# Kernel optimization log

Measured on AMD Instinct MI355X. Metric: run time of the kernel, lower is better.

Reference implementation:

```python
import jax, jax.numpy as jnp
import numpy as np

D_MODEL = 768
N_HEADS = 24
D_HEAD = 64
D_STATE = 64
CHUNK = 64
D_INNER = N_HEADS * D_HEAD  # 1536
N_LAYER = 24
B_SZ = 2
SEQ = 8192
RMS_EPS = 1.1920929e-07  # torch.finfo(float32).eps (nn.RMSNorm default eps)


def setup_inputs() -> dict:
    key = jax.random.key(0)
    ks = jax.random.split(key, 8)
    proj = N_HEADS * (1 + 2 * D_STATE)
    return {
        "hidden_states": jax.random.normal(ks[0], (B_SZ, SEQ, D_MODEL), jnp.float32),
        "norm_w": jnp.ones((D_MODEL,), jnp.float32),
        "in_proj_w": jax.random.normal(ks[1], (2 * D_INNER, D_MODEL), jnp.float32) * 0.02,
        "in_proj_b": jnp.zeros((2 * D_INNER,), jnp.float32),
        "conv_w": jax.random.normal(ks[2], (D_INNER, 1, 4), jnp.float32) * 0.25,
        "conv_b": jnp.zeros((D_INNER,), jnp.float32),
        "x_proj_w": jax.random.normal(ks[3], (proj, D_INNER), jnp.float32) * 0.02,
        "x_proj_b": jnp.zeros((proj,), jnp.float32),
        "A_log": jnp.full((N_HEADS,), float(np.log(0.5)), jnp.float32),
        "log2_alpha_base": jnp.full((N_HEADS,), -0.15, jnp.float32),
        "log2_beta": jnp.zeros((N_HEADS,), jnp.float32),
        "surprise_ema": jnp.ones((N_HEADS,), jnp.float32),
        "out_proj_w": jax.random.normal(ks[4], (D_MODEL, D_INNER), jnp.float32) * 0.02,
        "out_proj_b": jnp.zeros((D_MODEL,), jnp.float32),
        "res_gate": jnp.full((1,), 1.0 / float(np.sqrt(2 * N_LAYER)), jnp.float32),
    }


def _block_forward(hidden_states, norm_w, in_proj_w, in_proj_b, conv_w, conv_b,
                   x_proj_w, x_proj_b, A_log, log2_alpha_base, log2_beta,
                   surprise_ema, out_proj_w, out_proj_b, res_gate):
    residual = hidden_states
    b, L, _ = hidden_states.shape

    # RMSNorm
    x = hidden_states * jax.lax.rsqrt(
        jnp.mean(hidden_states ** 2, axis=-1, keepdims=True) + RMS_EPS) * norm_w

    # in_proj, split x/z
    xz = hidden_states_proj = x @ in_proj_w.T + in_proj_b
    x, z = jnp.split(xz, 2, axis=-1)  # [b, L, d_inner] each

    # causal depthwise conv1d (kernel 4, padding 3, then truncate to L)
    xc = jnp.transpose(x, (0, 2, 1))  # [b, C, L]
    xc = jax.lax.conv_general_dilated(
        xc, conv_w, window_strides=(1,), padding=[(3, 3)],
        dimension_numbers=("NCH", "OIH", "NCH"), feature_group_count=D_INNER)
    xc = xc[:, :, :L] + conv_b[None, :, None]
    x = jax.nn.silu(jnp.transpose(xc, (0, 2, 1)))  # [b, L, d_inner]

    # x_proj -> dt, B, C
    xp = (x @ x_proj_w.T + x_proj_b).reshape(b, L, N_HEADS, 1 + 2 * D_STATE)
    dt = xp[..., 0]
    B_ssm = xp[..., 1:1 + D_STATE]
    C_ssm = xp[..., 1 + D_STATE:]
    B_ssm = B_ssm / jnp.maximum(jnp.linalg.norm(B_ssm, axis=-1, keepdims=True), 1e-12)
    C_ssm = C_ssm / jnp.maximum(jnp.linalg.norm(C_ssm, axis=-1, keepdims=True), 1e-12)

    A = jnp.clip(A_log, -2.3, -0.01)[None, None, :]  # [1,1,H]
    dt_scale = jnp.clip(jax.nn.softplus(jnp.clip(dt, -10.0, 10.0)), 0.01, 10.0)
    A = jnp.clip(A * dt_scale, -20.0, -0.001)  # [b, L, H]

    X = x.reshape(b, L, N_HEADS, D_HEAD)

    # ---- chunked surprise-gated SSD (L divisible by CHUNK) ----
    n = L // CHUNK
    X_t = X.reshape(b, n, CHUNK, N_HEADS, D_HEAD).transpose(0, 3, 1, 2, 4)      # b h n c d
    A_t = A.reshape(b, n, CHUNK, N_HEADS).transpose(0, 3, 1, 2)                 # b h n c
    B_t = B_ssm.reshape(b, n, CHUNK, N_HEADS, D_STATE).transpose(0, 3, 1, 2, 4) # b h n c s
    C_t = C_ssm.reshape(b, n, CHUNK, N_HEADS, D_STATE).transpose(0, 3, 1, 2, 4) # b h n c s

    BX = jnp.einsum("bhncs,bhncd->bhnsd", B_t, X_t)
    chunk_surprise = jnp.mean(BX ** 2, axis=(-1, -2))  # [b, h, n]

    # surprise gate (training=True: EMA updated first, no_grad)
    mean_s = jax.lax.stop_gradient(jnp.mean(chunk_surprise, axis=(0, 2)))
    ema = 0.99 * surprise_ema + 0.01 * mean_s
    normalized = chunk_surprise / (ema[None, :, None] + 1e-6)
    alpha_base = 1.0 - 2.0 ** jnp.clip(log2_alpha_base, -3.32, -0.015)  # [H]
    beta = 2.0 ** jnp.clip(log2_beta, -2.0, 2.0)                        # [H]
    boost_pos = jax.nn.relu(jnp.tanh(beta[None, :, None] * normalized))
    ab = alpha_base[None, :, None]
    alpha = jnp.clip(ab + (1.0 - ab) * boost_pos, 0.01, 0.999)          # [b, h, n]

    A_mod = A_t * (1.0 - alpha)[..., None]          # b h n c
    A_cs = jnp.cumsum(A_mod, axis=-1)               # b h n c

    # intra-chunk: L[i,j] = exp(cs_i - cs_j) for i >= j
    diff = A_cs[..., :, None] - A_cs[..., None, :]  # b h n c c
    mask = jnp.tril(jnp.ones((CHUNK, CHUNK), bool))
    Lmat = jnp.where(mask, jnp.exp(diff), 0.0)
    CB = jnp.einsum("bhnid,bhnjd->bhnij", C_t, B_t)
    Y_intra = jnp.einsum("bhnij,bhnjd->bhnid", Lmat * CB, X_t)

    # inter-chunk recurrence
    decay_chunk = jnp.exp(jnp.sum(A_mod, axis=-1))              # b h n
    decay_to_end = jnp.exp(A_cs[..., -1:] - A_cs)               # b h n c
    h_chunk_final = jnp.einsum("bhnc,bhncs,bhncd->bhnsd",
                               decay_to_end, B_t, X_t)           # b h n s d

    def step(carry, inp):
        d, hf = inp  # d: [b,h], hf: [b,h,s,d]
        new = d[..., None, None] * carry + hf
        return new, carry  # emit state BEFORE this chunk

    carry0 = jnp.zeros((b, N_HEADS, D_STATE, D_HEAD), X.dtype)
    _, h_inter = jax.lax.scan(
        step, carry0,
        (decay_chunk.transpose(2, 0, 1), h_chunk_final.transpose(2, 0, 1, 3, 4)))
    h_inter = h_inter.transpose(1, 2, 0, 3, 4)  # b h n s d

    decay_from_start = jnp.exp(A_cs)  # b h n c
    Y_inter = jnp.einsum("bhnis,bhnsp,bhni->bhnip", C_t, h_inter, decay_from_start)

    Y = (Y_intra + Y_inter).transpose(0, 2, 3, 1, 4).reshape(b, L, D_INNER)

    # gate + out proj + gated residual
    y = jnp.clip(Y, -100.0, 100.0) * jax.nn.sigmoid(z)
    out = jnp.clip(y @ out_proj_w.T + out_proj_b, -100.0, 100.0)
    return residual + out * res_gate


def reference(hidden_states, norm_w, in_proj_w, in_proj_b, conv_w, conv_b,
              x_proj_w, x_proj_b, A_log, log2_alpha_base, log2_beta,
              surprise_ema, out_proj_w, out_proj_b, res_gate):
    return _block_forward(hidden_states, norm_w, in_proj_w, in_proj_b, conv_w,
                          conv_b, x_proj_w, x_proj_b, A_log, log2_alpha_base,
                          log2_beta, surprise_ema, out_proj_w, out_proj_b, res_gate)
```

## Files before the change

### kernel.cpp

```cpp
#include <hip/hip_runtime.h>
#include <hip/hip_bf16.h>
#include <cstdint>
#include <cstddef>

#define L_SEQ   8192
#define DMODEL  768
#define NHEADS  24
#define DINNER  1536
#define NPROJ   3096
#define NPROJP  3200
#define NPROJ2  3264
#define HSTR    136
#define NTOK    16384
#define BT      8192
#define RMS_EPS 1.1920929e-07f

typedef __hip_bfloat16 bf16;
typedef __attribute__((ext_vector_type(8))) short bf8v;
typedef __attribute__((ext_vector_type(4))) float f4v;

__device__ __forceinline__ float clampf(float x, float lo, float hi) {
    return fminf(fmaxf(x, lo), hi);
}
__device__ __forceinline__ float bf2f(bf16 v) { return __bfloat162float(v); }
__device__ __forceinline__ bf16  f2bf(float v) { return __float2bfloat16(v); }
__device__ __forceinline__ short f2bs(float v) {
    bf16 b = __float2bfloat16(v);
    return *reinterpret_cast<short*>(&b);
}
__device__ __forceinline__ float bs2f(short v) {
    return __uint_as_float(((unsigned)(unsigned short)v) << 16);
}
__device__ __forceinline__ void st1(float* p, float v) { *p = v; }
__device__ __forceinline__ void st1(bf16* p, float v) { *p = f2bf(v); }
__device__ __forceinline__ void st4(bf16* p, float4 v) {
    p[0] = f2bf(v.x); p[1] = f2bf(v.y); p[2] = f2bf(v.z); p[3] = f2bf(v.w);
}

#define GLOAD16(gsrc, ldst) __builtin_amdgcn_global_load_lds( \
    (const __attribute__((address_space(1))) void*)(gsrc),    \
    (__attribute__((address_space(3))) void*)(ldst), 16, 0, 0)

__global__ __launch_bounds__(256) void k_cvt(const float* __restrict__ s,
                                             bf16* __restrict__ d, int n4) {
    int i = blockIdx.x * 256 + threadIdx.x;
    if (i < n4) {
        float4 v = *(const float4*)&s[i * 4];
        st4(&d[i * 4], v);
    }
}
__global__ __launch_bounds__(256) void k_zero(bf16* __restrict__ d, int n) {
    int i = blockIdx.x * 256 + threadIdx.x;
    if (i < n) d[i] = f2bf(0.f);
}

__global__ __launch_bounds__(256) void k_rmsnorm(const float* __restrict__ hs,
                                                 const float* __restrict__ w,
                                                 bf16* __restrict__ xn) {
    int t = blockIdx.x;
    const float* p = hs + (size_t)t * DMODEL;
    float s = 0.f;
    for (int i = threadIdx.x; i < DMODEL; i += 256) { float v = p[i]; s += v * v; }
    for (int off = 32; off; off >>= 1) s += __shfl_xor(s, off, 64);
    __shared__ float ws4[4];
    int lane = threadIdx.x & 63, wv = threadIdx.x >> 6;
    if (lane == 0) ws4[wv] = s;
    __syncthreads();
    s = ws4[0] + ws4[1] + ws4[2] + ws4[3];
    float r = 1.0f / sqrtf(s * (1.0f / DMODEL) + RMS_EPS);
    bf16* o = xn + (size_t)t * DMODEL;
    for (int i = threadIdx.x; i < DMODEL; i += 256) o[i] = f2bf(p[i] * r * w[i]);
}

template <typename TC, int EPI>
__global__ __launch_bounds__(256) void k_mgemm(const bf16* __restrict__ A,
                                               const bf16* __restrict__ B,
                                               const float* __restrict__ bias,
                                               TC* __restrict__ C,
                                               int M, int N, int K,
                                               const float* __restrict__ resid,
                                               const float* __restrict__ gatep) {
    __shared__ short As[2][128 * 32];
    __shared__ short Bs[2][128 * 32];
    int tid = threadIdx.x;
    int lane = tid & 63, w = tid >> 6;

    int gx = gridDim.x, gy = gridDim.y;
    int bid = blockIdx.y * gx + blockIdx.x;
    int xcd = bid & 7, idx = bid >> 3;
    int bys = gy >> 3;
    int gby = bys < 8 ? bys : 8;
    int sg  = idx / (gx * gby);
    int rem = idx - sg * (gx * gby);
    int bx  = rem / gby;
    int byl = rem - bx * gby;
    int by  = xcd * bys + sg * gby + byl;
    int m0 = by * 128, n0 = bx * 128;

    int wm = (w >> 1) << 6, wn = (w & 1) << 6;

    const size_t rowskip = (size_t)16 * K * 2;
    const char* Ag = (const char*)(A + (size_t)(m0 + (w << 5) + (lane >> 2)) * K) + (lane & 3) * 16;
    const char* Bg = (const char*)(B + (size_t)(n0 + (w << 5) + (lane >> 2)) * K) + (lane & 3) * 16;
    short* Al0 = &As[0][(w << 5) * 32];
    short* Bl0 = &Bs[0][(w << 5) * 32];
    short* Al1 = &As[1][(w << 5) * 32];
    short* Bl1 = &Bs[1][(w << 5) * 32];

    f4v acc[4][4];
#pragma unroll
    for (int i = 0; i < 4; ++i)
#pragma unroll
        for (int j = 0; j < 4; ++j) acc[i][j] = (f4v){0.f, 0.f, 0.f, 0.f};

    auto stage = [&](int buf, int k0) {
        size_t kb = (size_t)k0 * 2;
        short* Al = buf ? Al1 : Al0;
        short* Bl = buf ? Bl1 : Bl0;
        GLOAD16(Ag + kb,           Al);
        GLOAD16(Ag + kb + rowskip, Al + 16 * 32);
        GLOAD16(Bg + kb,           Bl);
        GLOAD16(Bg + kb + rowskip, Bl + 16 * 32);
    };

    stage(0, 0);
    int cur = 0;
    int row16 = lane & 15, kg = (lane >> 4) << 3;
    for (int k0 = 0; k0 < K; k0 += 32) {
        __syncthreads();
        if (k0 + 32 < K) stage(cur ^ 1, k0 + 32);
        const short* Ab = As[cur];
        const short* Bb = Bs[cur];
        bf8v af[4], bfv[4];
#pragma unroll
        for (int fm = 0; fm < 4; ++fm)
            af[fm] = *(const bf8v*)&Ab[(wm + (fm << 4) + row16) * 32 + kg];
#pragma unroll
        for (int fn = 0; fn < 4; ++fn)
            bfv[fn] = *(const bf8v*)&Bb[(wn + (fn << 4) + row16) * 32 + kg];
#pragma unroll
        for (int fm = 0; fm < 4; ++fm)
#pragma unroll
            for (int fn = 0; fn < 4; ++fn)
                acc[fm][fn] = __builtin_amdgcn_mfma_f32_16x16x32_bf16(
                    af[fm], bfv[fn], acc[fm][fn], 0, 0, 0);
        cur ^= 1;
    }

    float gate = (EPI == 1) ? *gatep : 0.f;
    int rbase = m0 + wm + ((lane >> 4) << 2);
#pragma unroll
    for (int fn = 0; fn < 4; ++fn) {
        int col = n0 + wn + (fn << 4) + (lane & 15);
        if (col >= N) continue;
        float bc = bias[col];
        int dst = col;
        if (EPI == 2) {
            int hh = col / 129, q = col - hh * 129;
            dst = hh * HSTR + (q == 0 ? 0 : q + 7);
        }
#pragma unroll
        for (int fm = 0; fm < 4; ++fm) {
#pragma unroll
            for (int r = 0; r < 4; ++r) {
                int row = rbase + (fm << 4) + r;
                float v = acc[fm][fn][r] + bc;
                if (EPI == 1) {
                    v = resid[(size_t)row * N + col] + clampf(v, -100.f, 100.f) * gate;
                    st1(&C[(size_t)row * N + col], v);
                } else if (EPI == 2) {
                    st1(&C[(size_t)row * NPROJ2 + dst], v);
                } else {
                    st1(&C[(size_t)row * N + col], v);
                }
            }
        }
    }
}

__global__ __launch_bounds__(192) void k_conv8(const bf16* __restrict__ x,
                                               const float* __restrict__ cw,
                                               const float* __restrict__ cb,
                                               bf16* __restrict__ xc) {
    int c0 = threadIdx.x * 8;
    int r  = blockIdx.x;
    float acc[8];
#pragma unroll
    for (int j = 0; j < 8; ++j) acc[j] = cb[c0 + j];
#pragma unroll
    for (int k = 0; k < 4; ++k) {
        int lp = r - 3 + k;
        if (lp < 0) continue;
        bf8v v = *(const bf8v*)(const void*)(x + (size_t)lp * DINNER + c0);
#pragma unroll
        for (int j = 0; j < 8; ++j)
            acc[j] += cw[(c0 + j) * 4 + k] * bs2f(v[j]);
    }
    bf8v o;
#pragma unroll
    for (int j = 0; j < 8; ++j) {
        float a = acc[j];
        o[j] = f2bs(a / (1.f + expf(-a)));
    }
    *(bf8v*)(xc + (size_t)r * DINNER + c0) = o;
}

__global__ __launch_bounds__(256) void k_prep(const bf16* __restrict__ xp,
                                              const float* __restrict__ A_log,
                                              float* __restrict__ Aarr,
                                              float* __restrict__ invB,
                                              float* __restrict__ invC) {
    int wv = threadIdx.x >> 6, lane = threadIdx.x & 63;
    int idx = blockIdx.x * 4 + wv;
    int t = idx / 24, h = idx - t * 24;
    const bf16* base = xp + (size_t)t * NPROJ2 + h * HSTR;
    float b = bf2f(base[8 + lane]), c = bf2f(base[72 + lane]);
    float sb = b * b, sc = c * c;
    for (int off = 32; off; off >>= 1) {
        sb += __shfl_xor(sb, off, 64);
        sc += __shfl_xor(sc, off, 64);
    }
    if (lane == 0) {
        invB[idx] = 1.f / fmaxf(sqrtf(sb), 1e-12f);
        invC[idx] = 1.f / fmaxf(sqrtf(sc), 1e-12f);
        float dt = clampf(bf2f(base[0]), -10.f, 10.f);
        float dts = clampf(log1pf(expf(dt)), 0.01f, 10.f);
        float A = clampf(A_log[h], -2.3f, -0.01f) * dts;
        Aarr[idx] = clampf(A, -20.f, -0.001f);
    }
}

__global__ __launch_bounds__(256) void k_surprise_all(const bf16* __restrict__ xp,
                                                      const bf16* __restrict__ xc,
                                                      const float* __restrict__ invB,
                                                      float* __restrict__ cs) {
    int g = blockIdx.x;
    int cg = g / 24, h = g - cg * 24;
    int b = cg >> 7, nl = cg & 127;
    int t0 = cg * 64;
    size_t cs_idx = (size_t)(b * 24 + h) * 128 + nl;
    __shared__ short Ws[64 * 72];
    __shared__ short Xt[64 * 72];
    int tid = threadIdx.x;
#pragma unroll
    for (int half = 0; half < 2; ++half) {
        int tau = tid + half * 256;
        int c = tau >> 3, s0 = (tau & 7) << 3;
        int t = t0 + c;
        float ib = invB[t * 24 + h];
        bf8v Bv = *(const bf8v*)(const void*)(xp + (size_t)t * NPROJ2 + h * HSTR + 8 + s0);
        bf8v Xv = *(const bf8v*)(const void*)(xc + (size_t)t * DINNER + h * 64 + s0);
#pragma unroll
        for (int u = 0; u < 8; ++u) {
            Ws[(s0 + u) * 72 + c] = f2bs(bs2f(Bv[u]) * ib);
            Xt[(s0 + u) * 72 + c] = Xv[u];
        }
    }
    __syncthreads();
    int w = tid >> 6, lane = tid & 63;
    int r16 = lane & 15, kq = (lane >> 4) << 3;
    int strip = w << 4;
    f4v acc[4];
#pragma unroll
    for (int dt = 0; dt < 4; ++dt) acc[dt] = (f4v){0.f, 0.f, 0.f, 0.f};
#pragma unroll
    for (int ks = 0; ks < 2; ++ks) {
        bf8v af = *(const bf8v*)&Ws[(strip + r16) * 72 + ks * 32 + kq];
#pragma unroll
        for (int dt = 0; dt < 4; ++dt) {
            bf8v bf_ = *(const bf8v*)&Xt[((dt << 4) + r16) * 72 + ks * 32 + kq];
            acc[dt] = __builtin_amdgcn_mfma_f32_16x16x32_bf16(af, bf_, acc[dt], 0, 0, 0);
        }
    }
    float ss = 0.f;
#pragma unroll
    for (int dt = 0; dt < 4; ++dt)
#pragma unroll
        for (int r = 0; r < 4; ++r) ss += acc[dt][r] * acc[dt][r];
    for (int off = 32; off; off >>= 1) ss += __shfl_xor(ss, off, 64);
    __shared__ float ws4[4];
    if (lane == 0) ws4[w] = ss;
    __syncthreads();
    if (tid == 0) cs[cs_idx] = (ws4[0] + ws4[1] + ws4[2] + ws4[3]) * (1.f / 4096.f);
}

__global__ __launch_bounds__(256) void k_alpha(const float* __restrict__ cs,
                                               const float* __restrict__ ema0,
                                               const float* __restrict__ l2ab,
                                               const float* __restrict__ l2b,
                                               float* __restrict__ alpha) {
    int h = blockIdx.x, tid = threadIdx.x;
    int b = tid >> 7, n = tid & 127;
    int gi = (b * 24 + h) * 128 + n;
    float v = cs[gi];
    float s = v;
    for (int off = 32; off; off >>= 1) s += __shfl_xor(s, off, 64);
    __shared__ float ws4[4];
    int lane = tid & 63, wv = tid >> 6;
    if (lane == 0) ws4[wv] = s;
    __syncthreads();
    float total = ws4[0] + ws4[1] + ws4[2] + ws4[3];
    float ema = 0.99f * ema0[h] + 0.01f * (total * (1.f / 256.f));
    float ab = 1.f - exp2f(clampf(l2ab[h], -3.32f, -0.015f));
    float beta = exp2f(clampf(l2b[h], -2.f, 2.f));
    float nz = v / (ema + 1e-6f);
    float boost = fmaxf(tanhf(beta * nz), 0.f);
    alpha[gi] = clampf(ab + (1.f - ab) * boost, 0.01f, 0.999f);
}

__global__ __launch_bounds__(256) void k_chunk(const bf16* __restrict__ xp,
                                               const bf16* __restrict__ xc,
                                               const float* __restrict__ invB,
                                               const float* __restrict__ invC,
                                               const float* __restrict__ Aarr,
                                               const float* __restrict__ alpha,
                                               bf16* __restrict__ ybuf,
                                               bf16* __restrict__ hf,
                                               float* __restrict__ dchunk,
                                               int b) {
    int g = blockIdx.x;
    int h = g >> 7, nl = g & 127;
    int t0 = nl * 64;
    size_t gidx = (size_t)(b * 24 + h) * 128 + nl;
    size_t hbase = (size_t)g * 4096;
    float alp = alpha[gidx];
    __shared__ short Cs[64 * 72];
    __shared__ short Bs[64 * 72];
    __shared__ short Ws[64 * 72];
    __shared__ short Xt[64 * 72];
    __shared__ float Acs[64];
    __shared__ float dte[64];
    int tid = threadIdx.x;
    if (tid < 64) {
        float a = Aarr[(size_t)(t0 + tid) * 24 + h] * (1.f - alp);
        for (int off = 1; off < 64; off <<= 1) {
            float u = __shfl_up(a, off, 64);
            if (tid >= off) a += u;
        }
        Acs[tid] = a;
        float total = __shfl(a, 63, 64);
        dte[tid] = expf(total - a);
        if (tid == 0) dchunk[gidx] = expf(total);
    }
    __syncthreads();
#pragma unroll
    for (int half = 0; half < 2; ++half) {
        int tau = tid + half * 256;
        int c = tau >> 3, s0 = (tau & 7) << 3;
        int t = t0 + c;
        const bf16* bp = xp + (size_t)t * NPROJ2 + h * HSTR;
        float ib = invB[t * 24 + h], ic2 = invC[t * 24 + h];
        float dc = dte[c];
        bf8v Bv = *(const bf8v*)(const void*)(bp + 8 + s0);
        bf8v Cv = *(const bf8v*)(const void*)(bp + 72 + s0);
        bf8v Xv = *(const bf8v*)(const void*)(xc + (size_t)t * DINNER + h * 64 + s0);
        bf8v Bsc, Csc;
#pragma unroll
        for (int u = 0; u < 8; ++u) {
            float bv = bs2f(Bv[u]) * ib;
            Bsc[u] = f2bs(bv);
            Csc[u] = f2bs(bs2f(Cv[u]) * ic2);
            Ws[(s0 + u) * 72 + c] = f2bs(bv * dc);
            Xt[(s0 + u) * 72 + c] = Xv[u];
        }
        *(bf8v*)&Bs[c * 72 + s0] = Bsc;
        *(bf8v*)&Cs[c * 72 + s0] = Csc;
    }
    __syncthreads();
    int w = tid >> 6, lane = tid & 63;
    int r16 = lane & 15, kq = (lane >> 4) << 3;
    int strip = w << 4;
    f4v acb[4], ach[4];
#pragma unroll
    for (int jt = 0; jt < 4; ++jt) {
        acb[jt] = (f4v){0.f, 0.f, 0.f, 0.f};
        ach[jt] = (f4v){0.f, 0.f, 0.f, 0.f};
    }
#pragma unroll
    for (int ks = 0; ks < 2; ++ks) {
        bf8v afc = *(const bf8v*)&Cs[(strip + r16) * 72 + ks * 32 + kq];
        bf8v afw = *(const bf8v*)&Ws[(strip + r16) * 72 + ks * 32 + kq];
#pragma unroll
        for (int jt = 0; jt < 4; ++jt) {
            bf8v bb = *(const bf8v*)&Bs[((jt << 4) + r16) * 72 + ks * 32 + kq];
            acb[jt] = __builtin_amdgcn_mfma_f32_16x16x32_bf16(afc, bb, acb[jt], 0, 0, 0);
            bf8v xx = *(const bf8v*)&Xt[((jt << 4) + r16) * 72 + ks * 32 + kq];
            ach[jt] = __builtin_amdgcn_mfma_f32_16x16x32_bf16(afw, xx, ach[jt], 0, 0, 0);
        }
    }
    int rbase = strip + ((lane >> 4) << 2);
#pragma unroll
    for (int dt = 0; dt < 4; ++dt) {
        int d = (dt << 4) + r16;
#pragma unroll
        for (int r = 0; r < 4; ++r)
            hf[hbase + (size_t)(rbase + r) * 64 + d] = f2bf(ach[dt][r]);
    }
    __syncthreads();
    short* Ms = Cs;
#pragma unroll
    for (int jt = 0; jt < 4; ++jt) {
        int j = (jt << 4) + r16;
        float aj = Acs[j];
#pragma unroll
        for (int r = 0; r < 4; ++r) {
            int i = rbase + r;
            float m = (j <= i) ? expf(Acs[i] - aj) * acb[jt][r] : 0.f;
            Ms[i * 72 + j] = f2bs(m);
        }
    }
    __syncthreads();
    f4v acy[4];
#pragma unroll
    for (int dt = 0; dt < 4; ++dt) acy[dt] = (f4v){0.f, 0.f, 0.f, 0.f};
#pragma unroll
    for (int ks = 0; ks < 2; ++ks) {
        bf8v afm = *(const bf8v*)&Ms[(strip + r16) * 72 + ks * 32 + kq];
#pragma unroll
        for (int dt = 0; dt < 4; ++dt) {
            bf8v xx = *(const bf8v*)&Xt[((dt << 4) + r16) * 72 + ks * 32 + kq];
            acy[dt] = __builtin_amdgcn_mfma_f32_16x16x32_bf16(afm, xx, acy[dt], 0, 0, 0);
        }
    }
#pragma unroll
    for (int dt = 0; dt < 4; ++dt) {
        int d = (dt << 4) + r16;
#pragma unroll
        for (int r = 0; r < 4; ++r) {
            int i = rbase + r;
            ybuf[(size_t)(t0 + i) * DINNER + h * 64 + d] = f2bf(acy[dt][r]);
        }
    }
}

__global__ __launch_bounds__(256) void k_scan(bf16* __restrict__ hf,
                                              const float* __restrict__ dchunk,
                                              int b) {
    int h = blockIdx.x >> 4;
    int e = ((blockIdx.x & 15) << 8) + threadIdx.x;
    size_t abase = (size_t)h * 128 * 4096 + e;
    const float* dcp = dchunk + (size_t)(b * 24 + h) * 128;
    float c = 0.f;
    float v0 = bf2f(hf[abase]);
    float v1 = bf2f(hf[abase + 1 * 4096]);
    float v2 = bf2f(hf[abase + 2 * 4096]);
    float v3 = bf2f(hf[abase + 3 * 4096]);
    for (int nl = 0; nl < 128; nl += 4) {
        float p0 = (nl + 4 < 128) ? bf2f(hf[abase + (size_t)(nl + 4) * 4096]) : 0.f;
        float p1 = (nl + 5 < 128) ? bf2f(hf[abase + (size_t)(nl + 5) * 4096]) : 0.f;
        float p2 = (nl + 6 < 128) ? bf2f(hf[abase + (size_t)(nl + 6) * 4096]) : 0.f;
        float p3 = (nl + 7 < 128) ? bf2f(hf[abase + (size_t)(nl + 7) * 4096]) : 0.f;
        hf[abase + (size_t)nl * 4096] = f2bf(c);
        c = dcp[nl] * c + v0;
        hf[abase + (size_t)(nl + 1) * 4096] = f2bf(c);
        c = dcp[nl + 1] * c + v1;
        hf[abase + (size_t)(nl + 2) * 4096] = f2bf(c);
        c = dcp[nl + 2] * c + v2;
        hf[abase + (size_t)(nl + 3) * 4096] = f2bf(c);
        c = dcp[nl + 3] * c + v3;
        v0 = p0; v1 = p1; v2 = p2; v3 = p3;
    }
}

__global__ __launch_bounds__(256) void k_inter(const bf16* __restrict__ xp,
                                               const float* __restrict__ invC,
                                               const float* __restrict__ Aarr,
                                               const float* __restrict__ alpha,
                                               const bf16* __restrict__ hf,
                                               const bf16* __restrict__ zbuf,
                                               bf16* __restrict__ ybuf,
                                               int b) {
    int g = blockIdx.x;
    int h = g >> 7, nl = g & 127;
    int t0 = nl * 64;
    size_t gidx = (size_t)(b * 24 + h) * 128 + nl;
    size_t hbase = (size_t)g * 4096;
    float alp = alpha[gidx];
    __shared__ short Cs[64 * 72];
    __shared__ short Ht[64 * 72];
    __shared__ float dfs[64];
    int tid = threadIdx.x;
    if (tid < 64) {
        float a = Aarr[(size_t)(t0 + tid) * 24 + h] * (1.f - alp);
        for (int off = 1; off < 64; off <<= 1) {
            float u = __shfl_up(a, off, 64);
            if (tid >= off) a += u;
        }
        dfs[tid] = expf(a);
    }
#pragma unroll
    for (int half = 0; half < 2; ++half) {
        int tau = tid + half * 256;
        int c = tau >> 3, s0 = (tau & 7) << 3;
        int t = t0 + c;
        float ic2 = invC[t * 24 + h];
        bf8v Cv = *(const bf8v*)(const void*)(xp + (size_t)t * NPROJ2 + h * HSTR + 72 + s0);
        bf8v Hv = *(const bf8v*)(const void*)(hf + hbase + (size_t)c * 64 + s0);
        bf8v Csc;
#pragma unroll
        for (int u = 0; u < 8; ++u) {
            Csc[u] = f2bs(bs2f(Cv[u]) * ic2);
            Ht[(s0 + u) * 72 + c] = Hv[u];
        }
        *(bf8v*)&Cs[c * 72 + s0] = Csc;
    }
    __syncthreads();
    int w = tid >> 6, lane = tid & 63;
    int r16 = lane & 15, kq = (lane >> 4) << 3;
    int strip = w << 4;
    f4v acc[4];
#pragma unroll
    for (int dt = 0; dt < 4; ++dt) acc[dt] = (f4v){0.f, 0.f, 0.f, 0.f};
#pragma unroll
    for (int ks = 0; ks < 2; ++ks) {
        bf8v af = *(const bf8v*)&Cs[(strip + r16) * 72 + ks * 32 + kq];
#pragma unroll
        for (int dt = 0; dt < 4; ++dt) {
            bf8v hfr = *(const bf8v*)&Ht[((dt << 4) + r16) * 72 + ks * 32 + kq];
            acc[dt] = __builtin_amdgcn_mfma_f32_16x16x32_bf16(af, hfr, acc[dt], 0, 0, 0);
        }
    }
    int ibase = strip + ((lane >> 4) << 2);
#pragma unroll
    for (int dt = 0; dt < 4; ++dt) {
        int d = (dt << 4) + r16;
#pragma unroll
        for (int r = 0; r < 4; ++r) {
            int i = ibase + r;
            float df = dfs[i];
            size_t yoff = (size_t)(t0 + i) * DINNER + h * 64 + d;
            float Y = clampf(bf2f(ybuf[yoff]) + df * acc[dt][r], -100.f, 100.f);
            float zz = bf2f(zbuf[yoff]);
            ybuf[yoff] = f2bf(Y / (1.f + expf(-zz)));
        }
    }
}

extern "C" void kernel_launch(void* const* d_in, const int* in_sizes, int n_in,
                              void* d_out, int out_size, void* d_ws, size_t ws_size,
                              hipStream_t stream) {
    const float* hs     = (const float*)d_in[0];
    const float* norm_w = (const float*)d_in[1];
    const float* w1     = (const float*)d_in[2];
    const float* b1     = (const float*)d_in[3];
    const float* cw     = (const float*)d_in[4];
    const float* cbias  = (const float*)d_in[5];
    const float* w2     = (const float*)d_in[6];
    const float* b2     = (const float*)d_in[7];
    const float* A_log  = (const float*)d_in[8];
    const float* l2ab   = (const float*)d_in[9];
    const float* l2b    = (const float*)d_in[10];
    const float* ema0   = (const float*)d_in[11];
    const float* w3     = (const float*)d_in[12];
    const float* b3     = (const float*)d_in[13];
    const float* rg     = (const float*)d_in[14];
    float* out = (float*)d_out;

    char* base = (char*)d_ws;
    size_t off = 0;
    auto alloc = [&](size_t bytes) -> void* {
        void* p = base + off;
        off += (bytes + 255) & ~(size_t)255;
        return p;
    };
    bf16* w1bf  = (bf16*)alloc((size_t)2 * DINNER * DMODEL * 2);
    bf16* w2bf  = (bf16*)alloc((size_t)NPROJP * DINNER * 2);
    bf16* w3bf  = (bf16*)alloc((size_t)DMODEL * DINNER * 2);
    bf16* xnb   = (bf16*)alloc((size_t)BT * DMODEL * 2);
    bf16* ybuf  = (bf16*)alloc((size_t)BT * DINNER * 2);
    bf16* hf    = (bf16*)alloc((size_t)NHEADS * 128 * 4096 * 2);
    float* cs   = (float*)alloc((size_t)6144 * 4);
    float* alp  = (float*)alloc((size_t)6144 * 4);
    float* dch  = (float*)alloc((size_t)6144 * 4);
    bf16* xp    = (bf16*)alloc((size_t)NTOK * NPROJ2 * 2);
    float* Aarr = (float*)alloc((size_t)NTOK * 24 * 4);
    float* invB = (float*)alloc((size_t)NTOK * 24 * 4);
    float* invC = (float*)alloc((size_t)NTOK * 24 * 4);
    bf16* xbuf  = ybuf;
    bf16* xc_all = (bf16*)d_out;

    {
        int n1 = 2 * DINNER * DMODEL / 4, n2 = NPROJ * DINNER / 4, n3 = DMODEL * DINNER / 4;
        k_cvt<<<(n1 + 255) / 256, 256, 0, stream>>>(w1, w1bf, n1);
        k_cvt<<<(n2 + 255) / 256, 256, 0, stream>>>(w2, w2bf, n2);
        k_cvt<<<(n3 + 255) / 256, 256, 0, stream>>>(w3, w3bf, n3);
        int nz = (NPROJP - NPROJ) * DINNER;
        k_zero<<<(nz + 255) / 256, 256, 0, stream>>>(w2bf + (size_t)NPROJ * DINNER, nz);
    }

    const dim3 gXb(DINNER / 128, BT / 128);
    const dim3 gOb(DMODEL / 128, BT / 128);
    const dim3 gPall(NPROJP / 128, NTOK / 128);

    for (int bt = 0; bt < 2; ++bt) {
        size_t t0 = (size_t)bt * BT;
        k_rmsnorm<<<BT, 256, 0, stream>>>(hs + t0 * DMODEL, norm_w, xnb);
        k_mgemm<bf16, 0><<<gXb, 256, 0, stream>>>(xnb, w1bf, b1, xbuf,
                                                  BT, DINNER, DMODEL, nullptr, nullptr);
        k_conv8<<<BT, 192, 0, stream>>>(xbuf, cw, cbias, xc_all + t0 * DINNER);
    }
    k_mgemm<bf16, 2><<<gPall, 256, 0, stream>>>(xc_all, w2bf, b2, xp,
                                                NTOK, NPROJ, DINNER, nullptr, nullptr);
    k_prep<<<NTOK * 24 / 4, 256, 0, stream>>>(xp, A_log, Aarr, invB, invC);
    k_surprise_all<<<6144, 256, 0, stream>>>(xp, xc_all, invB, cs);
    k_alpha<<<24, 256, 0, stream>>>(cs, ema0, l2ab, l2b, alp);

    for (int pass = 0; pass < 2; ++pass) {
        int bt = 1 - pass;
        size_t t0 = (size_t)bt * BT;
        bf16* xc = xc_all + t0 * DINNER;
        bf16* zseg = xc;
        const bf16* xpS = xp + t0 * NPROJ2;
        const float* AarrS = Aarr + t0 * 24;
        const float* invBS = invB + t0 * 24;
        const float* invCS = invC + t0 * 24;
        k_chunk<<<NHEADS * 128, 256, 0, stream>>>(xpS, xc, invBS, invCS, AarrS, alp,
                                                  ybuf, hf, dch, bt);
        if (bt == 0)
            k_rmsnorm<<<BT, 256, 0, stream>>>(hs + t0 * DMODEL, norm_w, xnb);
        k_mgemm<bf16, 0><<<gXb, 256, 0, stream>>>(xnb, w1bf + (size_t)DINNER * DMODEL,
                                                  b1 + DINNER, zseg,
                                                  BT, DINNER, DMODEL, nullptr, nullptr);
        k_scan<<<384, 256, 0, stream>>>(hf, dch, bt);
        k_inter<<<NHEADS * 128, 256, 0, stream>>>(xpS, invCS, AarrS, alp, hf, zseg, ybuf, bt);
        k_mgemm<float, 1><<<gOb, 256, 0, stream>>>(ybuf, w3bf, b3, out + t0 * DMODEL,
                                                   BT, DMODEL, DINNER,
                                                   hs + t0 * DMODEL, rg);
    }
}
```

Measured before the change: 914.7 us.

## Compact x_proj output layout, split dt into small GEMM, conv four rows per block

The projected B/C buffer drops its padded per-head stride of 136 and uses a dense 128-per-head layout with a row stride of 3072. The dt column is no longer stored by the main projection GEMM. Instead a separate small GEMM over a gathered, zero-padded weight matrix writes dt to its own buffer, and the prep and chunk kernels index the new layout. The depthwise conv now computes four output rows per block from seven loaded input rows and hoists the weight loads, cutting redundant global reads. The trade-off is an extra GEMM launch: it covers only 24 useful columns padded to 128, so most of its tile compute is wasted and it runs with low occupancy.

```diff
diff --git a/kernel.cpp b/kernel.cpp
--- a/kernel.cpp
+++ b/kernel.cpp
@@ -9,8 +9,7 @@
 #define DINNER  1536
 #define NPROJ   3096
 #define NPROJP  3200
-#define NPROJ2  3264
-#define HSTR    136
+#define XPS     3072
 #define NTOK    16384
 #define BT      8192
 #define RMS_EPS 1.1920929e-07f
@@ -52,6 +51,17 @@
 __global__ __launch_bounds__(256) void k_zero(bf16* __restrict__ d, int n) {
     int i = blockIdx.x * 256 + threadIdx.x;
     if (i < n) d[i] = f2bf(0.f);
+}
+__global__ __launch_bounds__(256) void k_wdt(const float* __restrict__ w2,
+                                             const float* __restrict__ b2,
+                                             bf16* __restrict__ wdt,
+                                             float* __restrict__ bdt) {
+    int i = blockIdx.x * 256 + threadIdx.x;
+    if (i < 128 * DINNER) {
+        int h = i / DINNER, c = i - h * DINNER;
+        wdt[i] = f2bf(h < 24 ? w2[(size_t)(h * 129) * DINNER + c] : 0.f);
+    }
+    if (i < 128) bdt[i] = (i < 24) ? b2[i * 129] : 0.f;
 }
 
 __global__ __launch_bounds__(256) void k_rmsnorm(const float* __restrict__ hs,
@@ -157,7 +167,8 @@
         int dst = col;
         if (EPI == 2) {
             int hh = col / 129, q = col - hh * 129;
-            dst = hh * HSTR + (q == 0 ? 0 : q + 7);
+            if (q == 0) continue;
+            dst = hh * 128 + q - 1;
         }
 #pragma unroll
         for (int fm = 0; fm < 4; ++fm) {
@@ -169,7 +180,7 @@
                     v = resid[(size_t)row * N + col] + clampf(v, -100.f, 100.f) * gate;
                     st1(&C[(size_t)row * N + col], v);
                 } else if (EPI == 2) {
-                    st1(&C[(size_t)row * NPROJ2 + dst], v);
+                    st1(&C[(size_t)row * XPS + dst], v);
                 } else {
                     st1(&C[(size_t)row * N + col], v);
                 }
@@ -178,34 +189,42 @@
     }
 }
 
-__global__ __launch_bounds__(192) void k_conv8(const bf16* __restrict__ x,
+__global__ __launch_bounds__(192) void k_conv4(const bf16* __restrict__ x,
                                                const float* __restrict__ cw,
                                                const float* __restrict__ cb,
                                                bf16* __restrict__ xc) {
     int c0 = threadIdx.x * 8;
-    int r  = blockIdx.x;
-    float acc[8];
-#pragma unroll
-    for (int j = 0; j < 8; ++j) acc[j] = cb[c0 + j];
-#pragma unroll
-    for (int k = 0; k < 4; ++k) {
-        int lp = r - 3 + k;
-        if (lp < 0) continue;
-        bf8v v = *(const bf8v*)(const void*)(x + (size_t)lp * DINNER + c0);
-#pragma unroll
-        for (int j = 0; j < 8; ++j)
-            acc[j] += cw[(c0 + j) * 4 + k] * bs2f(v[j]);
-    }
-    bf8v o;
+    int r0 = blockIdx.x * 4;
+    bf8v xr[7];
+    const bf8v z8 = (bf8v){0, 0, 0, 0, 0, 0, 0, 0};
+#pragma unroll
+    for (int j = 0; j < 7; ++j) {
+        int rr = r0 - 3 + j;
+        xr[j] = (rr >= 0) ? *(const bf8v*)(const void*)(x + (size_t)rr * DINNER + c0) : z8;
+    }
+    float wk[4][8], cbv[8];
 #pragma unroll
     for (int j = 0; j < 8; ++j) {
-        float a = acc[j];
-        o[j] = f2bs(a / (1.f + expf(-a)));
-    }
-    *(bf8v*)(xc + (size_t)r * DINNER + c0) = o;
+        cbv[j] = cb[c0 + j];
+#pragma unroll
+        for (int k = 0; k < 4; ++k) wk[k][j] = cw[(c0 + j) * 4 + k];
+    }
+#pragma unroll
+    for (int i = 0; i < 4; ++i) {
+        bf8v o;
+#pragma unroll
+        for (int j = 0; j < 8; ++j) {
+            float a = cbv[j];
+#pragma unroll
+            for (int k = 0; k < 4; ++k) a += wk[k][j] * bs2f(xr[i + k][j]);
+            o[j] = f2bs(a / (1.f + expf(-a)));
+        }
+        *(bf8v*)(xc + (size_t)(r0 + i) * DINNER + c0) = o;
+    }
 }
 
 __global__ __launch_bounds__(256) void k_prep(const bf16* __restrict__ xp,
+                                              const bf16* __restrict__ dtb,
                                               const float* __restrict__ A_log,
                                               float* __restrict__ Aarr,
                                               float* __restrict__ invB,
@@ -213,8 +232,8 @@
     int wv = threadIdx.x >> 6, lane = threadIdx.x & 63;
     int idx = blockIdx.x * 4 + wv;
     int t = idx / 24, h = idx - t * 24;
-    const bf16* base = xp + (size_t)t * NPROJ2 + h * HSTR;
-    float b = bf2f(base[8 + lane]), c = bf2f(base[72 + lane]);
+    const bf16* base = xp + (size_t)t * XPS + h * 128;
+    float b = bf2f(base[lane]), c = bf2f(base[64 + lane]);
     float sb = b * b, sc = c * c;
     for (int off = 32; off; off >>= 1) {
         sb += __shfl_xor(sb, off, 64);
@@ -223,7 +242,7 @@
     if (lane == 0) {
         invB[idx] = 1.f / fmaxf(sqrtf(sb), 1e-12f);
         invC[idx] = 1.f / fmaxf(sqrtf(sc), 1e-12f);
-        float dt = clampf(bf2f(base[0]), -10.f, 10.f);
+        float dt = clampf(bf2f(dtb[idx]), -10.f, 10.f);
         float dts = clampf(log1pf(expf(dt)), 0.01f, 10.f);
         float A = clampf(A_log[h], -2.3f, -0.01f) * dts;
         Aarr[idx] = clampf(A, -20.f, -0.001f);
@@ -248,7 +267,7 @@
         int c = tau >> 3, s0 = (tau & 7) << 3;
         int t = t0 + c;
         float ib = invB[t * 24 + h];
-        bf8v Bv = *(const bf8v*)(const void*)(xp + (size_t)t * NPROJ2 + h * HSTR + 8 + s0);
+        bf8v Bv = *(const bf8v*)(const void*)(xp + (size_t)t * XPS + h * 128 + s0);
         bf8v Xv = *(const bf8v*)(const void*)(xc + (size_t)t * DINNER + h * 64 + s0);
 #pragma unroll
         for (int u = 0; u < 8; ++u) {
@@ -348,11 +367,11 @@
         int tau = tid + half * 256;
         int c = tau >> 3, s0 = (tau & 7) << 3;
         int t = t0 + c;
-        const bf16* bp = xp + (size_t)t * NPROJ2 + h * HSTR;
+        const bf16* bp = xp + (size_t)t * XPS + h * 128;
         float ib = invB[t * 24 + h], ic2 = invC[t * 24 + h];
         float dc = dte[c];
-        bf8v Bv = *(const bf8v*)(const void*)(bp + 8 + s0);
-        bf8v Cv = *(const bf8v*)(const void*)(bp + 72 + s0);
+        bf8v Bv = *(const bf8v*)(const void*)(bp + s0);
+        bf8v Cv = *(const bf8v*)(const void*)(bp + 64 + s0);
         bf8v Xv = *(const bf8v*)(const void*)(xc + (size_t)t * DINNER + h * 64 + s0);
         bf8v Bsc, Csc;
 #pragma unroll
@@ -494,7 +513,7 @@
         int c = tau >> 3, s0 = (tau & 7) << 3;
         int t = t0 + c;
         float ic2 = invC[t * 24 + h];
-        bf8v Cv = *(const bf8v*)(const void*)(xp + (size_t)t * NPROJ2 + h * HSTR + 72 + s0);
+        bf8v Cv = *(const bf8v*)(const void*)(xp + (size_t)t * XPS + h * 128 + 64 + s0);
         bf8v Hv = *(const bf8v*)(const void*)(hf + hbase + (size_t)c * 64 + s0);
         bf8v Csc;
 #pragma unroll
@@ -566,13 +585,16 @@
     bf16* w1bf  = (bf16*)alloc((size_t)2 * DINNER * DMODEL * 2);
     bf16* w2bf  = (bf16*)alloc((size_t)NPROJP * DINNER * 2);
     bf16* w3bf  = (bf16*)alloc((size_t)DMODEL * DINNER * 2);
+    bf16* wdt   = (bf16*)alloc((size_t)128 * DINNER * 2);
+    float* bdt  = (float*)alloc((size_t)128 * 4);
     bf16* xnb   = (bf16*)alloc((size_t)BT * DMODEL * 2);
     bf16* ybuf  = (bf16*)alloc((size_t)BT * DINNER * 2);
     bf16* hf    = (bf16*)alloc((size_t)NHEADS * 128 * 4096 * 2);
+    bf16* dtb   = (bf16*)alloc((size_t)NTOK * 24 * 2);
     float* cs   = (float*)alloc((size_t)6144 * 4);
     float* alp  = (float*)alloc((size_t)6144 * 4);
     float* dch  = (float*)alloc((size_t)6144 * 4);
-    bf16* xp    = (bf16*)alloc((size_t)NTOK * NPROJ2 * 2);
+    bf16* xp    = (bf16*)alloc((size_t)NTOK * XPS * 2);
     float* Aarr = (float*)alloc((size_t)NTOK * 24 * 4);
     float* invB = (float*)alloc((size_t)NTOK * 24 * 4);
     float* invC = (float*)alloc((size_t)NTOK * 24 * 4);
@@ -586,22 +608,26 @@
         k_cvt<<<(n3 + 255) / 256, 256, 0, stream>>>(w3, w3bf, n3);
         int nz = (NPROJP - NPROJ) * DINNER;
         k_zero<<<(nz + 255) / 256, 256, 0, stream>>>(w2bf + (size_t)NPROJ * DINNER, nz);
+        k_wdt<<<(128 * DINNER + 255) / 256, 256, 0, stream>>>(w2, b2, wdt, bdt);
     }
 
     const dim3 gXb(DINNER / 128, BT / 128);
     const dim3 gOb(DMODEL / 128, BT / 128);
     const dim3 gPall(NPROJP / 128, NTOK / 128);
+    const dim3 gDt(1, NTOK / 128);
 
     for (int bt = 0; bt < 2; ++bt) {
         size_t t0 = (size_t)bt * BT;
         k_rmsnorm<<<BT, 256, 0, stream>>>(hs + t0 * DMODEL, norm_w, xnb);
         k_mgemm<bf16, 0><<<gXb, 256, 0, stream>>>(xnb, w1bf, b1, xbuf,
                                                   BT, DINNER, DMODEL, nullptr, nullptr);
-        k_conv8<<<BT, 192, 0, stream>>>(xbuf, cw, cbias, xc_all + t0 * DINNER);
+        k_conv4<<<BT / 4, 192, 0, stream>>>(xbuf, cw, cbias, xc_all + t0 * DINNER);
     }
     k_mgemm<bf16, 2><<<gPall, 256, 0, stream>>>(xc_all, w2bf, b2, xp,
                                                 NTOK, NPROJ, DINNER, nullptr, nullptr);
-    k_prep<<<NTOK * 24 / 4, 256, 0, stream>>>(xp, A_log, Aarr, invB, invC);
+    k_mgemm<bf16, 0><<<gDt, 256, 0, stream>>>(xc_all, wdt, bdt, dtb,
+                                              NTOK, 24, DINNER, nullptr, nullptr);
+    k_prep<<<NTOK * 24 / 4, 256, 0, stream>>>(xp, dtb, A_log, Aarr, invB, invC);
     k_surprise_all<<<6144, 256, 0, stream>>>(xp, xc_all, invB, cs);
     k_alpha<<<24, 256, 0, stream>>>(cs, ema0, l2ab, l2b, alp);
 
@@ -610,7 +636,7 @@
         size_t t0 = (size_t)bt * BT;
         bf16* xc = xc_all + t0 * DINNER;
         bf16* zseg = xc;
-        const bf16* xpS = xp + t0 * NPROJ2;
+        const bf16* xpS = xp + t0 * XPS;
         const float* AarrS = Aarr + t0 * 24;
         const float* invBS = invB + t0 * 24;
         const float* invCS = invC + t0 * 24;
```

After: 784.1 us. -14.3%, faster.
